# Optimization experiments

Measured on AMD Instinct MI355X. Metric: run time of the kernel, lower is better.

Reference implementation:

```python
import jax, jax.numpy as jnp
import numpy as np
import math

N, C, CI, S, T, V = 64, 128, 32, 3, 64, 25  # batch, channels, inter_channels, num_subset, num_frame, num_node
EPS = 1e-5


def _make_pe(channel, joint_num, time_len, domain):
    # Faithful PositionalEncoding: pos over (t, j) raster, sin on even ch, cos on odd ch -> (1, C, T, V)
    if domain == 'spatial':
        pos = np.tile(np.arange(joint_num), time_len)
    else:
        pos = np.repeat(np.arange(time_len), joint_num)
    position = pos[:, None].astype(np.float64)
    div = np.exp(np.arange(0, channel, 2, dtype=np.float64) * (-math.log(10000.0) / channel))
    pe = np.zeros((time_len * joint_num, channel))
    pe[:, 0::2] = np.sin(position * div)
    pe[:, 1::2] = np.cos(position * div)
    pe = pe.reshape(time_len, joint_num, channel).transpose(2, 0, 1)[None]
    return jnp.asarray(pe, jnp.float32)


def _c1(x, w, b):
    # 1x1 Conv2d == channel GEMM: x (N,Cin,T,V), w (Cout,Cin)
    return jnp.einsum('nctv,oc->notv', x, w) + b[None, :, None, None]


def _bn(x, g, b, m, v):
    # BatchNorm2d in eval mode with running stats
    inv = g * jax.lax.rsqrt(v + EPS)
    return (x - m[None, :, None, None]) * inv[None, :, None, None] + b[None, :, None, None]


def _lrelu(x):
    return jax.nn.leaky_relu(x, 0.1)


def setup_inputs() -> dict:
    key = jax.random.key(0)
    ks = iter(jax.random.split(key, 48))

    def nrm(shape, s=0.05):
        return jax.random.normal(next(ks), shape, jnp.float32) * s

    inp = {}
    inp['x'] = jax.random.normal(next(ks), (N, C, T, V), jnp.float32)
    inp['pe_s'] = _make_pe(C, V, T, 'spatial')
    inp['pe_t'] = _make_pe(C, V, T, 'temporal')
    # spatial attention branch
    inp['w_in_s'] = nrm((2 * S * CI, C)); inp['b_in_s'] = nrm((2 * S * CI,))
    inp['alphas'] = jnp.ones((1, S, 1, 1), jnp.float32)
    inp['att0s'] = jnp.full((1, S, V, V), 1.0 / V, jnp.float32)
    inp['w_out_s'] = nrm((C, S * C)); inp['b_out_s'] = nrm((C,))
    inp['w_ff_s'] = nrm((C, C)); inp['b_ff_s'] = nrm((C,))
    # temporal attention branch
    inp['w_in_t'] = nrm((2 * S * CI, C)); inp['b_in_t'] = nrm((2 * S * CI,))
    inp['alphat'] = jnp.ones((1, S, 1, 1), jnp.float32)
    inp['att0t'] = jnp.tile(jnp.eye(T, dtype=jnp.float32)[None, None], (1, S, 1, 1))
    inp['w_out_t'] = nrm((C, S * C)); inp['b_out_t'] = nrm((C,))
    inp['w_ff_t'] = nrm((C, C)); inp['b_ff_t'] = nrm((C,))
    # BatchNorm (eval-mode) params for out_nets/ff_nets/out_nett/ff_nett
    for nm in ('out_s', 'ff_s', 'out_t', 'ff_t'):
        inp['g_' + nm] = 1.0 + nrm((C,))
        inp['be_' + nm] = nrm((C,))
        inp['m_' + nm] = nrm((C,), 0.1)
        inp['v_' + nm] = jax.random.uniform(next(ks), (C,), jnp.float32, 0.5, 1.5)
    return inp


def reference(x, pe_s, pe_t,
              w_in_s, b_in_s, alphas, att0s, w_out_s, b_out_s,
              w_ff_s, b_ff_s,
              w_in_t, b_in_t, alphat, att0t, w_out_t, b_out_t,
              w_ff_t, b_ff_t,
              g_out_s, be_out_s, m_out_s, v_out_s,
              g_ff_s, be_ff_s, m_ff_s, v_ff_s,
              g_out_t, be_out_t, m_out_t, v_out_t,
              g_ff_t, be_ff_t, m_ff_t, v_ff_t):
    n, c, t, v = x.shape
    s = alphas.shape[1]
    ci = w_in_s.shape[0] // (2 * s)
    # ---- spatial attention ----
    y = x + pe_s[:, :, :t]
    qk = _c1(y, w_in_s, b_in_s).reshape(n, 2 * s, ci, t, v)
    q, k = qk[:, :s], qk[:, s:]
    att_s = jnp.tanh(jnp.einsum('nsctu,nsctv->nsuv', q, k) / (ci * t)) * alphas + att0s
    y = jnp.einsum('nctu,nsuv->nsctv', x, att_s).reshape(n, s * c, t, v)
    y = _bn(_c1(y, w_out_s, b_out_s), g_out_s, be_out_s, m_out_s, v_out_s)
    y = _lrelu(x + y)  # downs1 == identity
    y2 = _bn(_c1(y, w_ff_s, b_ff_s), g_ff_s, be_ff_s, m_ff_s, v_ff_s)
    y = _lrelu(x + y2)  # downs2 == identity
    # ---- temporal attention ----
    z = y + pe_t[:, :, :t]
    qk = _c1(z, w_in_t, b_in_t).reshape(n, 2 * s, ci, t, v)
    q, k = qk[:, :s], qk[:, s:]
    att_t = jnp.tanh(jnp.einsum('nsctv,nscqv->nstq', q, k) / (ci * v)) * alphat + att0t
    z = jnp.einsum('nctv,nstq->nscqv', y, att_t).reshape(n, s * c, t, v)
    z = _bn(_c1(z, w_out_t, b_out_t), g_out_t, be_out_t, m_out_t, v_out_t)
    z = _lrelu(y + z)  # downt1 == identity
    z2 = _bn(_c1(z, w_ff_t, b_ff_t), g_ff_t, be_ff_t, m_ff_t, v_ff_t)
    z = _lrelu(y + z2)  # downt2 == identity
    return z
```

## Files before the change

kernel.cpp:

```cpp
#include <hip/hip_runtime.h>
#include <math.h>


#define EPS_ 1e-5f

typedef short bf16x8 __attribute__((ext_vector_type(8)));
typedef float f32x4 __attribute__((ext_vector_type(4)));

__device__ __forceinline__ unsigned short f2bf(float f) {
  unsigned u = __float_as_uint(f);
  unsigned r = u + 0x7fffu + ((u >> 16) & 1u);
  return (unsigned short)(r >> 16);
}
__device__ __forceinline__ float bf2f(unsigned short h) {
  return __uint_as_float((unsigned)h << 16);
}

struct SplitArgs {
  const float* src[6];
  unsigned short* dst[6];
  int K[6];
  int nfrag[6];
};
__global__ __launch_bounds__(64) void k_split_w(SplitArgs a) {
  const int mat = blockIdx.y;
  const int f = blockIdx.x;
  if (f >= a.nfrag[mat]) return;
  const int K = a.K[mat];
  const int ksteps = K >> 5;
  const int ot = f / ksteps, ks = f % ksteps;
  const int l = threadIdx.x;
  const float* sp = a.src[mat] + (size_t)(ot * 16 + (l & 15)) * K + ks * 32 + (l >> 4) * 8;
  float4 f0 = *(const float4*)sp;
  float4 f1 = *(const float4*)(sp + 4);
  float vals[8] = {f0.x, f0.y, f0.z, f0.w, f1.x, f1.y, f1.z, f1.w};
  unsigned short hi[8], lo[8];
#pragma unroll
  for (int j = 0; j < 8; ++j) {
    hi[j] = f2bf(vals[j]);
    lo[j] = f2bf(vals[j] - bf2f(hi[j]));
  }
  unsigned short* d = a.dst[mat] + (size_t)f * 1024 + l * 8;
  uint4 ph, pl;
  ph.x = hi[0] | ((unsigned)hi[1] << 16); ph.y = hi[2] | ((unsigned)hi[3] << 16);
  ph.z = hi[4] | ((unsigned)hi[5] << 16); ph.w = hi[6] | ((unsigned)hi[7] << 16);
  pl.x = lo[0] | ((unsigned)lo[1] << 16); pl.y = lo[2] | ((unsigned)lo[3] << 16);
  pl.z = lo[4] | ((unsigned)lo[5] << 16); pl.w = lo[6] | ((unsigned)lo[7] << 16);
  *(uint4*)d = ph;
  *(uint4*)(d + 512) = pl;
}

template <int KTOT, int OTOT, int EPI, int PT, bool HASPE>
__global__ __launch_bounds__(256 / PT) void k_conv_reg(
    const float* __restrict__ Yin, const float* __restrict__ pe,
    const unsigned short* __restrict__ WF, const float* __restrict__ bias,
    const float* __restrict__ g, const float* __restrict__ be,
    const float* __restrict__ bm, const float* __restrict__ bv,
    const float* __restrict__ res, float* __restrict__ out) {
  constexpr int KSTEPS = KTOT / 32;
  constexpr int OTILES = OTOT / 16;
  constexpr int WAVES = (256 / PT) / 64;
  const size_t yin_ns = (size_t)KTOT * 1600;
  const size_t out_ns = (size_t)OTOT * 1600;
  const int tid = threadIdx.x, lane = tid & 63, wv = tid >> 6;
  const int n = blockIdx.y;
  const int p0 = (blockIdx.x * WAVES + wv) * (PT * 16);
  const int krow = (lane >> 4) * 8;
  const float* Yb = Yin + (size_t)n * yin_ns;

  f32x4 acc[PT][OTILES];
#pragma unroll
  for (int pp = 0; pp < PT; ++pp)
#pragma unroll
    for (int ot = 0; ot < OTILES; ++ot) acc[pp][ot] = 0;

  float af[PT][8];
#pragma unroll
  for (int j = 0; j < 8; ++j) {
    const size_t ko = (size_t)(krow + j) * 1600;
#pragma unroll
    for (int pp = 0; pp < PT; ++pp) {
      const int pc = p0 + pp * 16 + (lane & 15);
      float v = Yb[ko + pc];
      if (HASPE) v += pe[ko + pc];
      af[pp][j] = v;
    }
  }

  for (int ks = 0; ks < KSTEPS; ++ks) {
    float an[PT][8];
    if (ks + 1 < KSTEPS) {
#pragma unroll
      for (int j = 0; j < 8; ++j) {
        const size_t ko = (size_t)((ks + 1) * 32 + krow + j) * 1600;
#pragma unroll
        for (int pp = 0; pp < PT; ++pp) {
          const int pc = p0 + pp * 16 + (lane & 15);
          float v = Yb[ko + pc];
          if (HASPE) v += pe[ko + pc];
          an[pp][j] = v;
        }
      }
    }
    bf16x8 ahi[PT], alo[PT];
#pragma unroll
    for (int pp = 0; pp < PT; ++pp) {
      union { unsigned u[4]; bf16x8 v; } ch, cl;
#pragma unroll
      for (int i = 0; i < 4; ++i) {
        const float fa = af[pp][2 * i], fb = af[pp][2 * i + 1];
        const unsigned ua = __float_as_uint(fa), ub = __float_as_uint(fb);
        ch.u[i] = (ua >> 16) | (ub & 0xffff0000u);
        const float ra = fa - __uint_as_float(ua & 0xffff0000u);
        const float rb = fb - __uint_as_float(ub & 0xffff0000u);
        cl.u[i] = (unsigned)f2bf(ra) | ((unsigned)f2bf(rb) << 16);
      }
      ahi[pp] = ch.v; alo[pp] = cl.v;
    }
#pragma unroll
    for (int ot = 0; ot < OTILES; ++ot) {
      const unsigned short* wp = WF + (size_t)(ot * KSTEPS + ks) * 1024 + (lane << 3);
      bf16x8 whi = *(const bf16x8*)wp;
      bf16x8 wlo = *(const bf16x8*)(wp + 512);
#pragma unroll
      for (int pp = 0; pp < PT; ++pp) {
        acc[pp][ot] = __builtin_amdgcn_mfma_f32_16x16x32_bf16(ahi[pp], whi, acc[pp][ot], 0, 0, 0);
        acc[pp][ot] = __builtin_amdgcn_mfma_f32_16x16x32_bf16(alo[pp], whi, acc[pp][ot], 0, 0, 0);
        acc[pp][ot] = __builtin_amdgcn_mfma_f32_16x16x32_bf16(ahi[pp], wlo, acc[pp][ot], 0, 0, 0);
      }
    }
    if (ks + 1 < KSTEPS) {
#pragma unroll
      for (int pp = 0; pp < PT; ++pp)
#pragma unroll
        for (int j = 0; j < 8; ++j) af[pp][j] = an[pp][j];
    }
  }

  const int o_l = lane & 15;
#pragma unroll
  for (int pp = 0; pp < PT; ++pp) {
    const int prow = p0 + pp * 16 + ((lane >> 4) << 2);
#pragma unroll
    for (int ot = 0; ot < OTILES; ++ot) {
      const int o = ot * 16 + o_l;
      f32x4 v = acc[pp][ot];
      if (EPI == 1) {
        const float inv = g[o] * rsqrtf(bv[o] + EPS_);
        const float beta = be[o] + (bias[o] - bm[o]) * inv;
        const f32x4 rv = *(const f32x4*)(res + (size_t)n * out_ns + (size_t)o * 1600 + prow);
#pragma unroll
        for (int j = 0; j < 4; ++j) {
          float val = v[j] * inv + beta + rv[j];
          v[j] = val > 0.f ? val : 0.1f * val;
        }
      } else {
        const float bo = bias[o];
#pragma unroll
        for (int j = 0; j < 4; ++j) v[j] += bo;
      }
      *(f32x4*)(out + (size_t)n * out_ns + (size_t)o * 1600 + prow) = v;
    }
  }
}

__global__ __launch_bounds__(256) void k_gram_s(
    const float* __restrict__ qk, const float* __restrict__ alphas,
    const float* __restrict__ att0, float* __restrict__ att) {
  const int s = blockIdx.x, n = blockIdx.y;
  const float* qb = qk + (size_t)(n * 6 + s) * 51200;
  const float* kb = qk + (size_t)(n * 6 + 3 + s) * 51200;
  __shared__ unsigned short Qhi[32][136], Qlo[32][136];
  __shared__ unsigned short Khi[32][136], Klo[32][136];
  const int tid = threadIdx.x;
  const int lane = tid & 63, wv = tid >> 6;
  const int mt = wv >> 1, nt = wv & 1;
  const int rowA = mt * 16 + (lane & 15);
  const int rowB = nt * 16 + (lane & 15);
  const int kg = (lane >> 4) * 8;
  f32x4 acc = 0;
  for (int kc = 0; kc < 16; ++kc) {
    for (int idx = tid; idx < 3200; idx += 256) {
      const int cp = idx / 1600, rem = idx - cp * 1600;
      const int t = rem / 25, u = rem - t * 25;
      const int kl = cp * 64 + t;
      float qv = qb[kc * 3200 + idx];
      float kv = kb[kc * 3200 + idx];
      unsigned short qh = f2bf(qv), kh = f2bf(kv);
      Qhi[u][kl] = qh; Qlo[u][kl] = f2bf(qv - bf2f(qh));
      Khi[u][kl] = kh; Klo[u][kl] = f2bf(kv - bf2f(kh));
    }
    __syncthreads();
#pragma unroll
    for (int ks = 0; ks < 4; ++ks) {
      bf16x8 qh = *(const bf16x8*)&Qhi[rowA][ks * 32 + kg];
      bf16x8 ql = *(const bf16x8*)&Qlo[rowA][ks * 32 + kg];
      bf16x8 kh = *(const bf16x8*)&Khi[rowB][ks * 32 + kg];
      bf16x8 kl = *(const bf16x8*)&Klo[rowB][ks * 32 + kg];
      acc = __builtin_amdgcn_mfma_f32_16x16x32_bf16(qh, kh, acc, 0, 0, 0);
      acc = __builtin_amdgcn_mfma_f32_16x16x32_bf16(ql, kh, acc, 0, 0, 0);
      acc = __builtin_amdgcn_mfma_f32_16x16x32_bf16(qh, kl, acc, 0, 0, 0);
    }
    __syncthreads();
  }
  const float al = alphas[s];
  float* ab = att + (size_t)(n * 3 + s) * 625;
  const int v = nt * 16 + (lane & 15);
  const int u0 = mt * 16 + ((lane >> 4) << 2);
  if (v < 25) {
#pragma unroll
    for (int j = 0; j < 4; ++j) {
      const int u = u0 + j;
      if (u < 25)
        ab[u * 25 + v] = tanhf(acc[j] * (1.0f / 2048.0f)) * al + att0[s * 625 + u * 25 + v];
    }
  }
}

__global__ __launch_bounds__(256) void k_gram_t(
    const float* __restrict__ qk, const float* __restrict__ alphat,
    const float* __restrict__ att0, float* __restrict__ att) {
  const int s = blockIdx.x, n = blockIdx.y;
  const float* qb = qk + (size_t)(n * 6 + s) * 51200;
  const float* kb = qk + (size_t)(n * 6 + 3 + s) * 51200;
  __shared__ unsigned short Qhi[64][136], Qlo[64][136];
  __shared__ unsigned short Khi[64][136], Klo[64][136];
  const int tid = threadIdx.x;
  const int lane = tid & 63, wv = tid >> 6;
  const int rowA = wv * 16 + (lane & 15);
  const int kg = (lane >> 4) * 8;
  for (int idx = tid; idx < 64 * 28; idx += 256) {
    const int t = idx / 28, r = idx - t * 28;
    const int col = (r / 7) * 32 + 25 + (r % 7);
    Qhi[t][col] = 0; Qlo[t][col] = 0; Khi[t][col] = 0; Klo[t][col] = 0;
  }
  f32x4 acc[4];
#pragma unroll
  for (int nt = 0; nt < 4; ++nt) acc[nt] = 0;
  for (int cc = 0; cc < 8; ++cc) {
    for (int idx = tid; idx < 6400; idx += 256) {
      const int cp = idx / 1600, rem = idx - cp * 1600;
      const int t = rem / 25, v = rem - t * 25;
      const int kl = cp * 32 + v;
      float qv = qb[cc * 6400 + idx];
      float kv = kb[cc * 6400 + idx];
      unsigned short qh = f2bf(qv), kh = f2bf(kv);
      Qhi[t][kl] = qh; Qlo[t][kl] = f2bf(qv - bf2f(qh));
      Khi[t][kl] = kh; Klo[t][kl] = f2bf(kv - bf2f(kh));
    }
    __syncthreads();
#pragma unroll
    for (int ks = 0; ks < 4; ++ks) {
      bf16x8 qh = *(const bf16x8*)&Qhi[rowA][ks * 32 + kg];
      bf16x8 ql = *(const bf16x8*)&Qlo[rowA][ks * 32 + kg];
#pragma unroll
      for (int nt = 0; nt < 4; ++nt) {
        const int rowB = nt * 16 + (lane & 15);
        bf16x8 kh = *(const bf16x8*)&Khi[rowB][ks * 32 + kg];
        bf16x8 kl = *(const bf16x8*)&Klo[rowB][ks * 32 + kg];
        acc[nt] = __builtin_amdgcn_mfma_f32_16x16x32_bf16(qh, kh, acc[nt], 0, 0, 0);
        acc[nt] = __builtin_amdgcn_mfma_f32_16x16x32_bf16(ql, kh, acc[nt], 0, 0, 0);
        acc[nt] = __builtin_amdgcn_mfma_f32_16x16x32_bf16(qh, kl, acc[nt], 0, 0, 0);
      }
    }
    __syncthreads();
  }
  const float al = alphat[s];
  float* ab = att + (size_t)(n * 3 + s) * 4096;
  const int t0 = wv * 16 + ((lane >> 4) << 2);
  const int qcol = lane & 15;
#pragma unroll
  for (int nt = 0; nt < 4; ++nt) {
#pragma unroll
    for (int j = 0; j < 4; ++j) {
      const int t = t0 + j, q = nt * 16 + qcol;
      ab[t * 64 + q] =
          tanhf(acc[nt][j] * (1.0f / 800.0f)) * al + att0[(size_t)s * 4096 + t * 64 + q];
    }
  }
}

__global__ __launch_bounds__(256) void k_apply_s(
    const float* __restrict__ x, const float* __restrict__ att,
    float* __restrict__ ya) {
  const int t = blockIdx.x, n = blockIdx.y;
  __shared__ float xs[128][25];
  __shared__ float al[1875];
  const float* xb = x + (size_t)n * 204800 + t * 25;
  for (int idx = threadIdx.x; idx < 3200; idx += 256)
    xs[idx / 25][idx % 25] = xb[(size_t)(idx / 25) * 1600 + idx % 25];
  for (int idx = threadIdx.x; idx < 1875; idx += 256)
    al[idx] = att[(size_t)n * 1875 + idx];
  __syncthreads();
  float* yb = ya + (size_t)n * 614400 + t * 25;
  for (int idx = threadIdx.x; idx < 9600; idx += 256) {
    const int s = idx / 3200, rem = idx - s * 3200;
    const int c = rem / 25, v = rem % 25;
    const float* ap = al + s * 625 + v;
    float a = 0.f;
#pragma unroll
    for (int u = 0; u < 25; ++u) a += xs[c][u] * ap[u * 25];
    yb[(size_t)(s * 128 + c) * 1600 + v] = a;
  }
}

__global__ __launch_bounds__(256) void k_apply_t(
    const float* __restrict__ y, const float* __restrict__ att,
    float* __restrict__ mid) {
  const int cg = blockIdx.x, n2 = blockIdx.y;
  __shared__ float ys[3200];
  const float* ybase = y + ((size_t)n2 * 128 + cg * 2) * 1600;
  for (int idx = threadIdx.x; idx < 3200; idx += 256) ys[idx] = ybase[idx];
  __syncthreads();
  const float* ab = att + (size_t)n2 * 3 * 4096;
  for (int item = threadIdx.x; item < 1200; item += 256) {
    const int s = item / 400, rem = item % 400, qg = rem / 25, v = rem % 25;
    const int q0 = qg * 4;
    const float* ap = ab + s * 4096 + q0;
    float acc[2][4] = {};
#pragma unroll 4
    for (int t = 0; t < 64; ++t) {
      float4 av = *(const float4*)(ap + t * 64);
      float y0 = ys[t * 25 + v];
      float y1 = ys[1600 + t * 25 + v];
      acc[0][0] += y0 * av.x; acc[0][1] += y0 * av.y; acc[0][2] += y0 * av.z; acc[0][3] += y0 * av.w;
      acc[1][0] += y1 * av.x; acc[1][1] += y1 * av.y; acc[1][2] += y1 * av.z; acc[1][3] += y1 * av.w;
    }
    float* mb = mid + (((size_t)n2 * 3 + s) * 128 + cg * 2) * 1600 + v;
#pragma unroll
    for (int ci = 0; ci < 2; ++ci)
#pragma unroll
      for (int qj = 0; qj < 4; ++qj)
        mb[(size_t)ci * 1600 + (q0 + qj) * 25] = acc[ci][qj];
  }
}

extern "C" void kernel_launch(void* const* d_in, const int* in_sizes, int n_in,
                              void* d_out, int out_size, void* d_ws, size_t ws_size,
                              hipStream_t stream) {
  const float* x       = (const float*)d_in[0];
  const float* pe_s    = (const float*)d_in[1];
  const float* pe_t    = (const float*)d_in[2];
  const float* w_in_s  = (const float*)d_in[3];
  const float* b_in_s  = (const float*)d_in[4];
  const float* alphas  = (const float*)d_in[5];
  const float* att0s   = (const float*)d_in[6];
  const float* w_out_s = (const float*)d_in[7];
  const float* b_out_s = (const float*)d_in[8];
  const float* w_ff_s  = (const float*)d_in[9];
  const float* b_ff_s  = (const float*)d_in[10];
  const float* w_in_t  = (const float*)d_in[11];
  const float* b_in_t  = (const float*)d_in[12];
  const float* alphat  = (const float*)d_in[13];
  const float* att0t   = (const float*)d_in[14];
  const float* w_out_t = (const float*)d_in[15];
  const float* b_out_t = (const float*)d_in[16];
  const float* w_ff_t  = (const float*)d_in[17];
  const float* b_ff_t  = (const float*)d_in[18];
  const float* g_out_s  = (const float*)d_in[19];
  const float* be_out_s = (const float*)d_in[20];
  const float* m_out_s  = (const float*)d_in[21];
  const float* v_out_s  = (const float*)d_in[22];
  const float* g_ff_s   = (const float*)d_in[23];
  const float* be_ff_s  = (const float*)d_in[24];
  const float* m_ff_s   = (const float*)d_in[25];
  const float* v_ff_s   = (const float*)d_in[26];
  const float* g_out_t  = (const float*)d_in[27];
  const float* be_out_t = (const float*)d_in[28];
  const float* m_out_t  = (const float*)d_in[29];
  const float* v_out_t  = (const float*)d_in[30];
  const float* g_ff_t   = (const float*)d_in[31];
  const float* be_ff_t  = (const float*)d_in[32];
  const float* m_ff_t   = (const float*)d_in[33];
  const float* v_ff_t   = (const float*)d_in[34];
  (void)in_sizes; (void)n_in; (void)out_size;

  float* ws = (float*)d_ws;
  float* OUT = (float*)d_out;
  const size_t NS = 204800;

  const bool full = ws_size >= (size_t)134938624;
  float* SCR;
  float* ATT;
  float* YB;
  unsigned short* WF;
  if (full) {
    SCR = ws; ATT = ws + 19660800; YB = ws + 20447232;
    WF = (unsigned short*)(ws + 33554432);
  } else {
    SCR = ws; ATT = ws + 4915200; YB = ws + 5701632;
    WF = (unsigned short*)(ws + 18808832);
  }

  SplitArgs sa;
  sa.src[0] = w_in_s;  sa.dst[0] = WF + 0;       sa.K[0] = 128; sa.nfrag[0] = 48;
  sa.src[1] = w_out_s; sa.dst[1] = WF + 49152;   sa.K[1] = 384; sa.nfrag[1] = 96;
  sa.src[2] = w_ff_s;  sa.dst[2] = WF + 147456;  sa.K[2] = 128; sa.nfrag[2] = 32;
  sa.src[3] = w_in_t;  sa.dst[3] = WF + 180224;  sa.K[3] = 128; sa.nfrag[3] = 48;
  sa.src[4] = w_out_t; sa.dst[4] = WF + 229376;  sa.K[4] = 384; sa.nfrag[4] = 96;
  sa.src[5] = w_ff_t;  sa.dst[5] = WF + 327680;  sa.K[5] = 128; sa.nfrag[5] = 32;
  k_split_w<<<dim3(96, 6), 64, 0, stream>>>(sa);

  dim3 blk(256), blk2(128);
  const float* nul = (const float*)0;

  if (full) {
    k_conv_reg<128, 192, 0, 1, true><<<dim3(25, 64), blk, 0, stream>>>(
        x, pe_s, WF + 0, b_in_s, nul, nul, nul, nul, nul, SCR);
    k_gram_s<<<dim3(3, 64), blk, 0, stream>>>(SCR, alphas, att0s, ATT);
    for (int h = 0; h < 2; ++h) {
      k_apply_s<<<dim3(64, 32), blk, 0, stream>>>(
          x + (size_t)h * 32 * NS, ATT + (size_t)h * 32 * 1875, SCR);
      k_conv_reg<384, 128, 1, 2, false><<<dim3(25, 32), blk2, 0, stream>>>(
          SCR, nul, WF + 49152, b_out_s, g_out_s, be_out_s, m_out_s, v_out_s,
          x + (size_t)h * 32 * NS, OUT + (size_t)h * 32 * NS);
    }
    k_conv_reg<128, 128, 1, 2, false><<<dim3(25, 64), blk2, 0, stream>>>(
        OUT, nul, WF + 147456, b_ff_s, g_ff_s, be_ff_s, m_ff_s, v_ff_s, x, YB);
    k_conv_reg<128, 192, 0, 1, true><<<dim3(25, 64), blk, 0, stream>>>(
        YB, pe_t, WF + 180224, b_in_t, nul, nul, nul, nul, nul, SCR);
    k_gram_t<<<dim3(3, 64), blk, 0, stream>>>(SCR, alphat, att0t, ATT);
    for (int h = 0; h < 2; ++h) {
      k_apply_t<<<dim3(64, 32), blk, 0, stream>>>(
          YB + (size_t)h * 32 * NS, ATT + (size_t)h * 32 * 12288, SCR);
      k_conv_reg<384, 128, 1, 2, false><<<dim3(25, 32), blk2, 0, stream>>>(
          SCR, nul, WF + 229376, b_out_t, g_out_t, be_out_t, m_out_t, v_out_t,
          YB + (size_t)h * 32 * NS, OUT + (size_t)h * 32 * NS);
    }
    k_conv_reg<128, 128, 1, 2, false><<<dim3(25, 64), blk2, 0, stream>>>(
        OUT, nul, WF + 327680, b_ff_t, g_ff_t, be_ff_t, m_ff_t, v_ff_t, YB, OUT);
  } else {
    for (int h = 0; h < 4; ++h) {
      k_conv_reg<128, 192, 0, 1, true><<<dim3(25, 16), blk, 0, stream>>>(
          x + (size_t)h * 16 * NS, pe_s, WF + 0, b_in_s, nul, nul, nul, nul, nul, SCR);
      k_gram_s<<<dim3(3, 16), blk, 0, stream>>>(SCR, alphas, att0s,
                                                ATT + (size_t)h * 16 * 1875);
    }
    for (int e = 0; e < 8; ++e) {
      k_apply_s<<<dim3(64, 8), blk, 0, stream>>>(
          x + (size_t)e * 8 * NS, ATT + (size_t)e * 8 * 1875, SCR);
      k_conv_reg<384, 128, 1, 2, false><<<dim3(25, 8), blk2, 0, stream>>>(
          SCR, nul, WF + 49152, b_out_s, g_out_s, be_out_s, m_out_s, v_out_s,
          x + (size_t)e * 8 * NS, OUT + (size_t)e * 8 * NS);
    }
    k_conv_reg<128, 128, 1, 2, false><<<dim3(25, 64), blk2, 0, stream>>>(
        OUT, nul, WF + 147456, b_ff_s, g_ff_s, be_ff_s, m_ff_s, v_ff_s, x, YB);
    for (int h = 0; h < 4; ++h) {
      k_conv_reg<128, 192, 0, 1, true><<<dim3(25, 16), blk, 0, stream>>>(
          YB + (size_t)h * 16 * NS, pe_t, WF + 180224, b_in_t, nul, nul, nul, nul, nul, SCR);
      k_gram_t<<<dim3(3, 16), blk, 0, stream>>>(SCR, alphat, att0t,
                                                ATT + (size_t)h * 16 * 12288);
    }
    for (int e = 0; e < 8; ++e) {
      k_apply_t<<<dim3(64, 8), blk, 0, stream>>>(
          YB + (size_t)e * 8 * NS, ATT + (size_t)e * 8 * 12288, SCR);
      k_conv_reg<384, 128, 1, 2, false><<<dim3(25, 8), blk2, 0, stream>>>(
          SCR, nul, WF + 229376, b_out_t, g_out_t, be_out_t, m_out_t, v_out_t,
          YB + (size_t)e * 8 * NS, OUT + (size_t)e * 8 * NS);
    }
    k_conv_reg<128, 128, 1, 2, false><<<dim3(25, 64), blk2, 0, stream>>>(
        OUT, nul, WF + 327680, b_ff_t, g_ff_t, be_ff_t, m_ff_t, v_ff_t, YB, OUT);
  }
}
```

Before: 895.6 us.

## Register-block spatial apply, split temporal apply by subset, retune out-conv blocks

The spatial apply kernel now stages attention into a padded shared array and has each thread compute four output nodes with float4 shared loads, reusing each x value across them. The temporal apply kernel gets a grid dimension for the subset, so each block stages one 64x64 attention matrix in shared memory instead of reading it from global memory. The output-projection convolutions switch to a different template parameter and 256-thread blocks. Together these cut shared and global memory traffic per output in the apply stages, at the cost of re-loading the y tile three times in the temporal apply and idle threads in its 400-item loop.

```diff
diff --git a/kernel.cpp b/kernel.cpp
--- a/kernel.cpp
+++ b/kernel.cpp
@@ -285,44 +285,60 @@
     float* __restrict__ ya) {
   const int t = blockIdx.x, n = blockIdx.y;
   __shared__ float xs[128][25];
-  __shared__ float al[1875];
+  __shared__ float al[3][25][28];
   const float* xb = x + (size_t)n * 204800 + t * 25;
   for (int idx = threadIdx.x; idx < 3200; idx += 256)
     xs[idx / 25][idx % 25] = xb[(size_t)(idx / 25) * 1600 + idx % 25];
-  for (int idx = threadIdx.x; idx < 1875; idx += 256)
-    al[idx] = att[(size_t)n * 1875 + idx];
+  const float* attb = att + (size_t)n * 1875;
+  for (int idx = threadIdx.x; idx < 1875; idx += 256) {
+    const int s = idx / 625, rem = idx - s * 625;
+    al[s][rem / 25][rem % 25] = attb[idx];
+  }
+  for (int idx = threadIdx.x; idx < 225; idx += 256) {
+    const int s = idx / 75, r = idx - s * 75;
+    al[s][r / 3][25 + r % 3] = 0.f;
+  }
   __syncthreads();
   float* yb = ya + (size_t)n * 614400 + t * 25;
-  for (int idx = threadIdx.x; idx < 9600; idx += 256) {
-    const int s = idx / 3200, rem = idx - s * 3200;
-    const int c = rem / 25, v = rem % 25;
-    const float* ap = al + s * 625 + v;
-    float a = 0.f;
-#pragma unroll
-    for (int u = 0; u < 25; ++u) a += xs[c][u] * ap[u * 25];
-    yb[(size_t)(s * 128 + c) * 1600 + v] = a;
+  for (int item = threadIdx.x; item < 2688; item += 256) {
+    const int s = item / 896, r = item - s * 896;
+    const int c = r / 7, vq = r - c * 7;
+    float a0 = 0.f, a1 = 0.f, a2 = 0.f, a3 = 0.f;
+#pragma unroll 5
+    for (int u = 0; u < 25; ++u) {
+      const float xv = xs[c][u];
+      const float4 q4 = *(const float4*)&al[s][u][vq * 4];
+      a0 += xv * q4.x; a1 += xv * q4.y; a2 += xv * q4.z; a3 += xv * q4.w;
+    }
+    float* dst = yb + (size_t)(s * 128 + c) * 1600 + vq * 4;
+    const int vrem = 25 - vq * 4;
+    dst[0] = a0;
+    if (vrem > 1) dst[1] = a1;
+    if (vrem > 2) dst[2] = a2;
+    if (vrem > 3) dst[3] = a3;
   }
 }
 
 __global__ __launch_bounds__(256) void k_apply_t(
     const float* __restrict__ y, const float* __restrict__ att,
     float* __restrict__ mid) {
-  const int cg = blockIdx.x, n2 = blockIdx.y;
+  const int cg = blockIdx.x, s = blockIdx.y, n2 = blockIdx.z;
   __shared__ float ys[3200];
+  __shared__ float at[4096];
   const float* ybase = y + ((size_t)n2 * 128 + cg * 2) * 1600;
   for (int idx = threadIdx.x; idx < 3200; idx += 256) ys[idx] = ybase[idx];
+  const float* ab = att + ((size_t)n2 * 3 + s) * 4096;
+  for (int idx = threadIdx.x; idx < 4096; idx += 256) at[idx] = ab[idx];
   __syncthreads();
-  const float* ab = att + (size_t)n2 * 3 * 4096;
-  for (int item = threadIdx.x; item < 1200; item += 256) {
-    const int s = item / 400, rem = item % 400, qg = rem / 25, v = rem % 25;
+  for (int item = threadIdx.x; item < 400; item += 256) {
+    const int qg = item / 25, v = item - qg * 25;
     const int q0 = qg * 4;
-    const float* ap = ab + s * 4096 + q0;
     float acc[2][4] = {};
 #pragma unroll 4
     for (int t = 0; t < 64; ++t) {
-      float4 av = *(const float4*)(ap + t * 64);
-      float y0 = ys[t * 25 + v];
-      float y1 = ys[1600 + t * 25 + v];
+      const float4 av = *(const float4*)&at[t * 64 + q0];
+      const float y0 = ys[t * 25 + v];
+      const float y1 = ys[1600 + t * 25 + v];
       acc[0][0] += y0 * av.x; acc[0][1] += y0 * av.y; acc[0][2] += y0 * av.z; acc[0][3] += y0 * av.w;
       acc[1][0] += y1 * av.x; acc[1][1] += y1 * av.y; acc[1][2] += y1 * av.z; acc[1][3] += y1 * av.w;
     }
@@ -411,7 +427,7 @@
     for (int h = 0; h < 2; ++h) {
       k_apply_s<<<dim3(64, 32), blk, 0, stream>>>(
           x + (size_t)h * 32 * NS, ATT + (size_t)h * 32 * 1875, SCR);
-      k_conv_reg<384, 128, 1, 2, false><<<dim3(25, 32), blk2, 0, stream>>>(
+      k_conv_reg<384, 128, 1, 1, false><<<dim3(25, 32), blk, 0, stream>>>(
           SCR, nul, WF + 49152, b_out_s, g_out_s, be_out_s, m_out_s, v_out_s,
           x + (size_t)h * 32 * NS, OUT + (size_t)h * 32 * NS);
     }
@@ -421,9 +437,9 @@
         YB, pe_t, WF + 180224, b_in_t, nul, nul, nul, nul, nul, SCR);
     k_gram_t<<<dim3(3, 64), blk, 0, stream>>>(SCR, alphat, att0t, ATT);
     for (int h = 0; h < 2; ++h) {
-      k_apply_t<<<dim3(64, 32), blk, 0, stream>>>(
+      k_apply_t<<<dim3(64, 3, 32), blk, 0, stream>>>(
           YB + (size_t)h * 32 * NS, ATT + (size_t)h * 32 * 12288, SCR);
-      k_conv_reg<384, 128, 1, 2, false><<<dim3(25, 32), blk2, 0, stream>>>(
+      k_conv_reg<384, 128, 1, 1, false><<<dim3(25, 32), blk, 0, stream>>>(
           SCR, nul, WF + 229376, b_out_t, g_out_t, be_out_t, m_out_t, v_out_t,
           YB + (size_t)h * 32 * NS, OUT + (size_t)h * 32 * NS);
     }
@@ -439,7 +455,7 @@
     for (int e = 0; e < 8; ++e) {
       k_apply_s<<<dim3(64, 8), blk, 0, stream>>>(
           x + (size_t)e * 8 * NS, ATT + (size_t)e * 8 * 1875, SCR);
-      k_conv_reg<384, 128, 1, 2, false><<<dim3(25, 8), blk2, 0, stream>>>(
+      k_conv_reg<384, 128, 1, 1, false><<<dim3(25, 8), blk, 0, stream>>>(
           SCR, nul, WF + 49152, b_out_s, g_out_s, be_out_s, m_out_s, v_out_s,
           x + (size_t)e * 8 * NS, OUT + (size_t)e * 8 * NS);
     }
@@ -452,9 +468,9 @@
                                                 ATT + (size_t)h * 16 * 12288);
     }
     for (int e = 0; e < 8; ++e) {
-      k_apply_t<<<dim3(64, 8), blk, 0, stream>>>(
+      k_apply_t<<<dim3(64, 3, 8), blk, 0, stream>>>(
           YB + (size_t)e * 8 * NS, ATT + (size_t)e * 8 * 12288, SCR);
-      k_conv_reg<384, 128, 1, 2, false><<<dim3(25, 8), blk2, 0, stream>>>(
+      k_conv_reg<384, 128, 1, 1, false><<<dim3(25, 8), blk, 0, stream>>>(
           SCR, nul, WF + 229376, b_out_t, g_out_t, be_out_t, m_out_t, v_out_t,
           YB + (size_t)e * 8 * NS, OUT + (size_t)e * 8 * NS);
     }
```

New measurement: 839.9 us. 1.07x faster.
